# Performance work log

Measured on AMD Instinct MI355X. Metric: run time of the kernel, lower is better.

The kernel has to match this reference:

```python
import jax, jax.numpy as jnp
import numpy as np

N = 100000      # nodes
E = 1_600_000   # edges (avg degree 16)
DIMS = [(64, 64), (64, 64), (64, 40)]  # gnn_layers [64,64,64,40]


def setup_inputs() -> dict:
    key = jax.random.key(0)
    ks = jax.random.split(key, 2 + 3 * len(DIMS))
    inp = {
        "x": jax.random.normal(ks[0], (N, DIMS[0][0]), jnp.float32),
        "edge_index": jax.random.randint(ks[1], (2, E), 0, N),
    }
    k = 2
    for i, (din, dout) in enumerate(DIMS):
        s = 1.0 / np.sqrt(din)
        inp[f"Wl{i}"] = jax.random.uniform(ks[k], (din, dout), jnp.float32, -s, s); k += 1
        inp[f"bl{i}"] = jax.random.uniform(ks[k], (dout,), jnp.float32, -s, s); k += 1
        inp[f"Wr{i}"] = jax.random.uniform(ks[k], (din, dout), jnp.float32, -s, s); k += 1
    return inp


def _sage_conv(x, src, dst, Wl, bl, Wr):
    # PyG SAGEConv (mean aggr): out = lin_l(mean_{j in N(i)} x_j) + lin_r(x_i)
    deg = jax.ops.segment_sum(jnp.ones((src.shape[0],), x.dtype), dst, num_segments=N)
    agg = jax.ops.segment_sum(x[src], dst, num_segments=N)  # [N, din] scatter-add
    agg = agg / jnp.clip(deg, 1.0)[:, None]                  # mean; isolated nodes -> 0
    return agg @ Wl + bl + x @ Wr


def reference(x, edge_index, Wl0, bl0, Wr0, Wl1, bl1, Wr1, Wl2, bl2, Wr2):
    src, dst = edge_index[0], edge_index[1]
    h = x
    params = [(Wl0, bl0, Wr0), (Wl1, bl1, Wr1), (Wl2, bl2, Wr2)]
    for i, (Wl, bl, Wr) in enumerate(params):
        h = _sage_conv(h, src, dst, Wl, bl, Wr)
        if i != len(params) - 1:
            h = jax.nn.relu(h)
            # F.dropout with training=False is identity (eval mode)
    return jax.nn.log_softmax(h, axis=1)
```

## Files before the change

kernel.cpp:

```cpp
#include <hip/hip_runtime.h>
#include <math.h>

#define ACT_RELU 0
#define ACT_LSM  1
#define BSH 8
#define MAXNB 512

typedef __attribute__((ext_vector_type(8))) short bf16x8;
typedef __attribute__((ext_vector_type(4))) float f32x4;
typedef __attribute__((ext_vector_type(2))) float f32x2;

__device__ __forceinline__ unsigned f2bf(float f) {
  unsigned u = __float_as_uint(f);
  u += 0x7fffu + ((u >> 16) & 1u);
  return u >> 16;
}
template <bool HI>
__device__ __forceinline__ f32x2 f8cvt(unsigned w) {
  return __builtin_amdgcn_cvt_pk_f32_fp8((int)w, HI);
}
__device__ __forceinline__ unsigned char f2f8(float v) {
  return (unsigned char)(__builtin_amdgcn_cvt_pk_fp8_f32(v, v, 0, false) & 0xff);
}

__global__ void k_zero(int* __restrict__ p, int n) {
  int i = blockIdx.x * 256 + threadIdx.x;
  if (i < n) p[i] = 0;
}

__global__ void k_histB(const int* __restrict__ dst, int* __restrict__ bucket_cnt,
                        int E, int NB) {
  __shared__ int cntL[MAXNB];
  int t = threadIdx.x;
  for (int b = t; b < NB; b += 256) cntL[b] = 0;
  __syncthreads();
  int e0 = blockIdx.x * 4096;
  int e1 = min(e0 + 4096, E);
  for (int i = e0 + t; i < e1; i += 256) atomicAdd(&cntL[dst[i] >> BSH], 1);
  __syncthreads();
  for (int b = t; b < NB; b += 256)
    if (cntL[b]) atomicAdd(&bucket_cnt[b], cntL[b]);
}

__global__ void k_bscan(const int* __restrict__ bucket_cnt, int* __restrict__ bucket_base,
                        int* __restrict__ bucket_cursor, int NB) {
  __shared__ int sm[MAXNB];
  int t = threadIdx.x;
  sm[t] = (t < NB) ? bucket_cnt[t] : 0;
  __syncthreads();
  for (int off = 1; off < MAXNB; off <<= 1) {
    int x = (t >= off) ? sm[t - off] : 0;
    __syncthreads();
    sm[t] += x;
    __syncthreads();
  }
  int ex = (t == 0) ? 0 : sm[t - 1];
  if (t <= NB) bucket_base[t] = ex;
  if (t < NB) bucket_cursor[t] = ex;
}

__global__ void k_partition(const int* __restrict__ src, const int* __restrict__ dst,
                            int* __restrict__ bucket_cursor, int2* __restrict__ tmp,
                            int E, int NB) {
  __shared__ int cntL[MAXNB];
  __shared__ int baseL[MAXNB];
  int t = threadIdx.x;
  for (int b = t; b < NB; b += 256) cntL[b] = 0;
  __syncthreads();
  int e0 = blockIdx.x * 4096;
  int e1 = min(e0 + 4096, E);
  for (int i = e0 + t; i < e1; i += 256) atomicAdd(&cntL[dst[i] >> BSH], 1);
  __syncthreads();
  for (int b = t; b < NB; b += 256) {
    int c = cntL[b];
    baseL[b] = c ? atomicAdd(&bucket_cursor[b], c) : 0;
    cntL[b] = 0;
  }
  __syncthreads();
  for (int i = e0 + t; i < e1; i += 256) {
    int s = src[i], d = dst[i];
    int b = d >> BSH;
    int r = atomicAdd(&cntL[b], 1);
    tmp[baseL[b] + r] = make_int2(s, d);
  }
}

__global__ void __launch_bounds__(256) k_bmake(const int2* __restrict__ tmp,
                                               const int* __restrict__ bucket_base,
                                               int* __restrict__ row_ptr,
                                               int* __restrict__ edge_src,
                                               int N, int E, int NB) {
  __shared__ int cntL[256];
  __shared__ int scanL[256];
  int b = blockIdx.x;
  int t = threadIdx.x;
  int e0 = bucket_base[b], e1 = bucket_base[b + 1];
  cntL[t] = 0;
  __syncthreads();
  for (int i = e0 + t; i < e1; i += 256) atomicAdd(&cntL[tmp[i].y & 255], 1);
  __syncthreads();
  int v = cntL[t];
  scanL[t] = v;
  __syncthreads();
  for (int off = 1; off < 256; off <<= 1) {
    int x = (t >= off) ? scanL[t - off] : 0;
    __syncthreads();
    scanL[t] += x;
    __syncthreads();
  }
  int exc = scanL[t] - v;
  int node = (b << BSH) + t;
  if (node < N) row_ptr[node] = e0 + exc;
  if (b == NB - 1 && t == 0) row_ptr[N] = E;
  __syncthreads();
  cntL[t] = e0 + exc;
  __syncthreads();
  for (int i = e0 + t; i < e1; i += 256) {
    int2 e = tmp[i];
    int p = atomicAdd(&cntL[e.y & 255], 1);
    edge_src[p] = e.x;
  }
}

__global__ void k_hist(const int* __restrict__ dst, int* __restrict__ cnt, int E) {
  int i = blockIdx.x * blockDim.x + threadIdx.x;
  if (i < E) atomicAdd(&cnt[dst[i]], 1);
}

__global__ void k_scan_part(const int* __restrict__ cnt, int* __restrict__ bsum, int M) {
  __shared__ int sm[256];
  int t = threadIdx.x;
  int base = blockIdx.x * 2048 + t * 8;
  int s = 0;
#pragma unroll
  for (int j = 0; j < 8; ++j) { int i = base + j; if (i < M) s += cnt[i]; }
  sm[t] = s;
  __syncthreads();
  for (int off = 128; off > 0; off >>= 1) {
    if (t < off) sm[t] += sm[t + off];
    __syncthreads();
  }
  if (t == 0) bsum[blockIdx.x] = sm[0];
}

__global__ void k_scan_mid(const int* __restrict__ bsum, int* __restrict__ boff, int nb) {
  int l = threadIdx.x;
  int v = (l < nb) ? bsum[l] : 0;
  int inc = v;
  for (int off = 1; off < 64; off <<= 1) {
    int u = __shfl_up(inc, off);
    if (l >= off) inc += u;
  }
  if (l < nb) boff[l] = inc - v;
}

__global__ void k_scan_final(const int* __restrict__ cnt, const int* __restrict__ boff,
                             int* __restrict__ row_ptr, int* __restrict__ cursor, int M) {
  __shared__ int sm[256];
  int t = threadIdx.x;
  int base = blockIdx.x * 2048 + t * 8;
  int v[8];
  int s = 0;
#pragma unroll
  for (int j = 0; j < 8; ++j) { int i = base + j; v[j] = (i < M) ? cnt[i] : 0; s += v[j]; }
  sm[t] = s;
  __syncthreads();
  for (int off = 1; off < 256; off <<= 1) {
    int x = (t >= off) ? sm[t - off] : 0;
    __syncthreads();
    sm[t] += x;
    __syncthreads();
  }
  int run = boff[blockIdx.x] + sm[t] - s;
#pragma unroll
  for (int j = 0; j < 8; ++j) {
    int i = base + j;
    if (i < M) { row_ptr[i] = run; cursor[i] = run; }
    run += v[j];
  }
}

__global__ void k_fill(const int* __restrict__ src, const int* __restrict__ dst,
                       int* __restrict__ cursor, int* __restrict__ edge_src, int E) {
  int i = blockIdx.x * blockDim.x + threadIdx.x;
  if (i < E) {
    int d = dst[i];
    int p = atomicAdd(&cursor[d], 1);
    edge_src[p] = src[i];
  }
}

__global__ void __launch_bounds__(256) k_cast(const float* __restrict__ x,
                                              unsigned short* __restrict__ xb,
                                              unsigned char* __restrict__ x8, int n) {
  int i = blockIdx.x * 256 + threadIdx.x;
  if (i * 8 < n) {
    const float4* p = (const float4*)(x + (size_t)i * 8);
    float4 a = p[0], b = p[1];
    uint4 w;
    w.x = f2bf(a.x) | (f2bf(a.y) << 16);
    w.y = f2bf(a.z) | (f2bf(a.w) << 16);
    w.z = f2bf(b.x) | (f2bf(b.y) << 16);
    w.w = f2bf(b.z) | (f2bf(b.w) << 16);
    *(uint4*)(xb + (size_t)i * 8) = w;
    uint2 q;
    q.x = (unsigned)__builtin_amdgcn_cvt_pk_fp8_f32(a.x, a.y, 0, false);
    q.x = (unsigned)__builtin_amdgcn_cvt_pk_fp8_f32(a.z, a.w, (int)q.x, true);
    q.y = (unsigned)__builtin_amdgcn_cvt_pk_fp8_f32(b.x, b.y, 0, false);
    q.y = (unsigned)__builtin_amdgcn_cvt_pk_fp8_f32(b.z, b.w, (int)q.y, true);
    *(uint2*)(x8 + (size_t)i * 8) = q;
  }
}

#define MPAD 80

template <int DOUT, int ACT>
__global__ void __launch_bounds__(256) k_layer(const unsigned short* __restrict__ h,
                                               const unsigned char* __restrict__ h8,
                                               const int* __restrict__ row_ptr,
                                               const int* __restrict__ edge_src,
                                               const float* __restrict__ Wl,
                                               const float* __restrict__ Wr,
                                               const float* __restrict__ bias,
                                               void* __restrict__ outv,
                                               unsigned char* __restrict__ out8, int n) {
  constexpr int NT = (DOUT + 15) / 16;
  constexpr int PADN = NT * 16;
  __shared__ unsigned short Wlds[128 * PADN];
  __shared__ unsigned short meanL[4][16 * MPAD];
  int t = threadIdx.x;

  for (int fi = t; fi < 128 * PADN; fi += 256) {
    int k7 = fi & 7;
    int kb = (fi >> 3) & 3;
    int c16 = (fi >> 5) & 15;
    int rest = fi >> 9;
    int nt = rest % NT;
    int kb5 = rest / NT;
    int k = kb5 * 32 + kb * 8 + k7;
    int nn = nt * 16 + c16;
    float v = 0.f;
    if (nn < DOUT) v = (k < 64) ? Wl[k * DOUT + nn] : Wr[(k - 64) * DOUT + nn];
    Wlds[fi] = (unsigned short)f2bf(v);
  }

  int w = t >> 6, lane = t & 63;
  int r0 = (blockIdx.x * 4 + w) * 16;
  int g = lane & 7;
  int lb = lane & ~7;

  for (int half = 0; half < 2; ++half) {
    int node = half * 8 + (lane >> 3);
    int i = r0 + node;
    float a[8];
#pragma unroll
    for (int c = 0; c < 8; ++c) a[c] = 0.f;
    float scale = 0.f;
    if (i < n) {
      int rp0 = row_ptr[i], rp1 = row_ptr[i + 1];
      int deg = rp1 - rp0;
      scale = (deg > 0) ? (1.0f / (float)deg) : 0.f;
      for (int base = 0; base < deg; base += 8) {
        int idx = rp0 + base + g;
        int sv = (idx < rp1) ? edge_src[idx] : 0;
        int cnt = min(8, deg - base);
        uint2 v0, v1, v2, v3, v4, v5, v6, v7;
#pragma unroll
        for (int e = 0; e < 8; ++e) {
          int s = __shfl(sv, lb | e);
          const uint2* p = (const uint2*)(h8 + (size_t)s * 64) + g;
          if (e == 0 && e < cnt) v0 = *p;
          if (e == 1 && e < cnt) v1 = *p;
          if (e == 2 && e < cnt) v2 = *p;
          if (e == 3 && e < cnt) v3 = *p;
          if (e == 4 && e < cnt) v4 = *p;
          if (e == 5 && e < cnt) v5 = *p;
          if (e == 6 && e < cnt) v6 = *p;
          if (e == 7 && e < cnt) v7 = *p;
        }
#define ACCUM(vv, ee)                                                    \
        if ((ee) < cnt) {                                                \
          f32x2 p0 = f8cvt<false>(vv.x), p1 = f8cvt<true>(vv.x);         \
          f32x2 p2 = f8cvt<false>(vv.y), p3 = f8cvt<true>(vv.y);         \
          a[0] += p0.x; a[1] += p0.y; a[2] += p1.x; a[3] += p1.y;        \
          a[4] += p2.x; a[5] += p2.y; a[6] += p3.x; a[7] += p3.y;        \
        }
        ACCUM(v0, 0) ACCUM(v1, 1) ACCUM(v2, 2) ACCUM(v3, 3)
        ACCUM(v4, 4) ACCUM(v5, 5) ACCUM(v6, 6) ACCUM(v7, 7)
#undef ACCUM
      }
    }
    uint4 wv;
    wv.x = f2bf(a[0] * scale) | (f2bf(a[1] * scale) << 16);
    wv.y = f2bf(a[2] * scale) | (f2bf(a[3] * scale) << 16);
    wv.z = f2bf(a[4] * scale) | (f2bf(a[5] * scale) << 16);
    wv.w = f2bf(a[6] * scale) | (f2bf(a[7] * scale) << 16);
    *(uint4*)&meanL[w][node * MPAD + g * 8] = wv;
  }
  __syncthreads();

  int c = lane & 15;
  int kb = lane >> 4;
  bf16x8 bf[4][NT];
#pragma unroll
  for (int s = 0; s < 4; ++s)
#pragma unroll
    for (int nt = 0; nt < NT; ++nt)
      bf[s][nt] = *(const bf16x8*)&Wlds[(((s * NT + nt) * 16 + c) * 4 + kb) * 8];

  bf16x8 af[4];
  af[0] = *(const bf16x8*)&meanL[w][c * MPAD + kb * 8];
  af[1] = *(const bf16x8*)&meanL[w][c * MPAD + 32 + kb * 8];
  int row = r0 + c;
  if (row >= n) row = n - 1;
  size_t rb = (size_t)row * 64 + kb * 8;
  af[2] = *(const bf16x8*)(h + rb);
  af[3] = *(const bf16x8*)(h + rb + 32);

  f32x4 acc[NT];
#pragma unroll
  for (int nt = 0; nt < NT; ++nt) acc[nt] = (f32x4){0.f, 0.f, 0.f, 0.f};
#pragma unroll
  for (int s = 0; s < 4; ++s)
#pragma unroll
    for (int nt = 0; nt < NT; ++nt)
      acc[nt] = __builtin_amdgcn_mfma_f32_16x16x32_bf16(af[s], bf[s][nt], acc[nt], 0, 0, 0);

  int rbase = r0 + kb * 4;
  if (ACT == ACT_RELU) {
    unsigned short* out = (unsigned short*)outv;
#pragma unroll
    for (int nt = 0; nt < NT; ++nt) {
      float bval = bias[nt * 16 + c];
#pragma unroll
      for (int r = 0; r < 4; ++r) {
        int R = rbase + r;
        if (R < n) {
          float v = fmaxf(acc[nt][r] + bval, 0.f);
          size_t o = (size_t)R * DOUT + nt * 16 + c;
          out[o] = (unsigned short)f2bf(v);
          out8[o] = f2f8(v);
        }
      }
    }
  } else {
    float* out = (float*)outv;
    float bv[NT];
#pragma unroll
    for (int nt = 0; nt < NT; ++nt) bv[nt] = ((nt * 16 + c) < DOUT) ? bias[nt * 16 + c] : 0.f;
#pragma unroll
    for (int r = 0; r < 4; ++r) {
      int R = rbase + r;
      float v[NT];
      float m = -INFINITY;
#pragma unroll
      for (int nt = 0; nt < NT; ++nt) {
        bool valid = (nt * 16 + c) < DOUT;
        v[nt] = valid ? (acc[nt][r] + bv[nt]) : -INFINITY;
        m = fmaxf(m, v[nt]);
      }
#pragma unroll
      for (int off = 1; off < 16; off <<= 1) m = fmaxf(m, __shfl_xor(m, off));
      float es = 0.f;
#pragma unroll
      for (int nt = 0; nt < NT; ++nt)
        if ((nt * 16 + c) < DOUT) es += expf(v[nt] - m);
#pragma unroll
      for (int off = 1; off < 16; off <<= 1) es += __shfl_xor(es, off);
      float lse = logf(es);
      if (R < n) {
#pragma unroll
        for (int nt = 0; nt < NT; ++nt)
          if ((nt * 16 + c) < DOUT) out[(size_t)R * DOUT + nt * 16 + c] = v[nt] - m - lse;
      }
    }
  }
}

extern "C" void kernel_launch(void* const* d_in, const int* in_sizes, int n_in,
                              void* d_out, int out_size, void* d_ws, size_t ws_size,
                              hipStream_t stream) {
  const float* x   = (const float*)d_in[0];
  const int*   ei  = (const int*)d_in[1];
  const float* Wl0 = (const float*)d_in[2];
  const float* bl0 = (const float*)d_in[3];
  const float* Wr0 = (const float*)d_in[4];
  const float* Wl1 = (const float*)d_in[5];
  const float* bl1 = (const float*)d_in[6];
  const float* Wr1 = (const float*)d_in[7];
  const float* Wl2 = (const float*)d_in[8];
  const float* bl2 = (const float*)d_in[9];
  const float* Wr2 = (const float*)d_in[10];
  float* out = (float*)d_out;

  int N = in_sizes[0] / 64;
  int E = in_sizes[1] / 2;
  int M = N + 1;
  int NB = (N + 255) >> BSH;
  const int* src = ei;
  const int* dst = ei + E;

  char* p = (char*)d_ws;
  auto alloc = [&](size_t bytes) {
    char* r = p;
    p += (bytes + 255) & ~(size_t)255;
    return r;
  };
  int* cnt      = (int*)alloc((size_t)M * 4);
  int* row_ptr  = (int*)alloc((size_t)M * 4);
  int* cursor   = (int*)alloc((size_t)M * 4);
  int* bsum     = (int*)alloc(256 * 4);
  int* boff     = (int*)alloc(256 * 4);
  int* bk_cnt   = (int*)alloc((MAXNB + 1) * 4);
  int* bk_base  = (int*)alloc((MAXNB + 1) * 4);
  int* bk_cur   = (int*)alloc((MAXNB + 1) * 4);
  int* edge_src = (int*)alloc((size_t)E * 4);
  size_t szR1 = (size_t)E * 8 > (size_t)N * 128 ? (size_t)E * 8 : (size_t)N * 128;
  char* R1              = alloc(szR1);
  unsigned short* hbA   = (unsigned short*)alloc((size_t)N * 128);
  unsigned char*  P8A   = (unsigned char*)alloc((size_t)N * 64);
  unsigned char*  P8B   = (unsigned char*)alloc((size_t)N * 64);
  if ((size_t)(p - (char*)d_ws) > ws_size) return;

  bool bucketed = (NB <= MAXNB);
  int eb4 = (E + 4095) / 4096;

  if (bucketed) {
    k_zero<<<(MAXNB + 256) / 256, 256, 0, stream>>>(bk_cnt, MAXNB + 1);
    k_histB<<<eb4, 256, 0, stream>>>(dst, bk_cnt, E, NB);
    k_bscan<<<1, MAXNB, 0, stream>>>(bk_cnt, bk_base, bk_cur, NB);
    k_partition<<<eb4, 256, 0, stream>>>(src, dst, bk_cur, (int2*)R1, E, NB);
    k_bmake<<<NB, 256, 0, stream>>>((const int2*)R1, bk_base, row_ptr, edge_src, N, E, NB);
  } else {
    k_zero<<<(M + 255) / 256, 256, 0, stream>>>(cnt, M);
    k_hist<<<(E + 255) / 256, 256, 0, stream>>>(dst, cnt, E);
    int nb = (M + 2047) / 2048;
    k_scan_part<<<nb, 256, 0, stream>>>(cnt, bsum, M);
    k_scan_mid<<<1, 64, 0, stream>>>(bsum, boff, nb);
    k_scan_final<<<nb, 256, 0, stream>>>(cnt, boff, row_ptr, cursor, M);
    k_fill<<<(E + 255) / 256, 256, 0, stream>>>(src, dst, cursor, edge_src, E);
  }

  unsigned short* xb  = (unsigned short*)R1;
  unsigned short* hbB = (unsigned short*)R1;
  unsigned char*  x8  = P8A;
  unsigned char*  h8A = P8B;
  unsigned char*  h8B = P8A;

  int cb = (N * 64 / 8 + 255) / 256;
  int gb = (N + 63) / 64;

  k_cast<<<cb, 256, 0, stream>>>(x, xb, x8, N * 64);
  k_layer<64, ACT_RELU><<<gb, 256, 0, stream>>>(xb, x8, row_ptr, edge_src, Wl0, Wr0, bl0, hbA, h8A, N);
  k_layer<64, ACT_RELU><<<gb, 256, 0, stream>>>(hbA, h8A, row_ptr, edge_src, Wl1, Wr1, bl1, hbB, h8B, N);
  k_layer<40, ACT_LSM><<<gb, 256, 0, stream>>>(hbB, h8B, row_ptr, edge_src, Wl2, Wr2, bl2, out, nullptr, N);
}
```

Measured before the change: 221.8 us.

## Split fp8 feature table into two 32-column planes and gather per plane

The fp8 copy of node features is stored as two planes of 32 columns each instead of 64-byte rows. The gather loop now has 4 lanes per node covering all 16 nodes at once, and it runs two passes, one per plane. Each gathered row is 32 bytes, so the random-access working set per pass is halved, which is meant to improve L2/MALL hit rates. Nontemporal hints are added to streaming loads and stores, at the cost of reading the edge list twice.

```diff
diff --git a/kernel.cpp b/kernel.cpp
--- a/kernel.cpp
+++ b/kernel.cpp
@@ -9,6 +9,8 @@
 typedef __attribute__((ext_vector_type(8))) short bf16x8;
 typedef __attribute__((ext_vector_type(4))) float f32x4;
 typedef __attribute__((ext_vector_type(2))) float f32x2;
+typedef __attribute__((ext_vector_type(4))) unsigned int u32x4;
+typedef __attribute__((ext_vector_type(2))) unsigned int u32x2;
 
 __device__ __forceinline__ unsigned f2bf(float f) {
   unsigned u = __float_as_uint(f);
@@ -192,23 +194,30 @@
 
 __global__ void __launch_bounds__(256) k_cast(const float* __restrict__ x,
                                               unsigned short* __restrict__ xb,
-                                              unsigned char* __restrict__ x8, int n) {
+                                              unsigned char* __restrict__ x8, int node_n,
+                                              int n) {
   int i = blockIdx.x * 256 + threadIdx.x;
   if (i * 8 < n) {
-    const float4* p = (const float4*)(x + (size_t)i * 8);
-    float4 a = p[0], b = p[1];
-    uint4 w;
+    const f32x4* p = (const f32x4*)(x + (size_t)i * 8);
+    f32x4 a = __builtin_nontemporal_load(p);
+    f32x4 b = __builtin_nontemporal_load(p + 1);
+    u32x4 w;
     w.x = f2bf(a.x) | (f2bf(a.y) << 16);
     w.y = f2bf(a.z) | (f2bf(a.w) << 16);
     w.z = f2bf(b.x) | (f2bf(b.y) << 16);
     w.w = f2bf(b.z) | (f2bf(b.w) << 16);
-    *(uint4*)(xb + (size_t)i * 8) = w;
-    uint2 q;
+    __builtin_nontemporal_store(w, (u32x4*)(xb + (size_t)i * 8));
+    u32x2 q;
     q.x = (unsigned)__builtin_amdgcn_cvt_pk_fp8_f32(a.x, a.y, 0, false);
     q.x = (unsigned)__builtin_amdgcn_cvt_pk_fp8_f32(a.z, a.w, (int)q.x, true);
     q.y = (unsigned)__builtin_amdgcn_cvt_pk_fp8_f32(b.x, b.y, 0, false);
     q.y = (unsigned)__builtin_amdgcn_cvt_pk_fp8_f32(b.z, b.w, (int)q.y, true);
-    *(uint2*)(x8 + (size_t)i * 8) = q;
+    int node = i >> 3;
+    int d0 = (i & 7) * 8;
+    int plane = d0 >> 5;
+    int off = d0 & 31;
+    __builtin_nontemporal_store(q,
+        (u32x2*)(x8 + (size_t)plane * node_n * 32 + (size_t)node * 32 + off));
   }
 }
 
@@ -246,56 +255,62 @@
 
   int w = t >> 6, lane = t & 63;
   int r0 = (blockIdx.x * 4 + w) * 16;
-  int g = lane & 7;
-  int lb = lane & ~7;
-
-  for (int half = 0; half < 2; ++half) {
-    int node = half * 8 + (lane >> 3);
-    int i = r0 + node;
+  int node = lane >> 2;
+  int g = lane & 3;
+  int nb = lane & ~3;
+  int i = r0 + node;
+
+  int rp0 = 0, rp1 = 0, deg = 0;
+  float scale = 0.f;
+  if (i < n) {
+    rp0 = row_ptr[i];
+    rp1 = row_ptr[i + 1];
+    deg = rp1 - rp0;
+    scale = (deg > 0) ? (1.0f / (float)deg) : 0.f;
+  }
+
+  for (int p = 0; p < 2; ++p) {
+    const unsigned char* hp = h8 + (size_t)p * n * 32;
     float a[8];
 #pragma unroll
     for (int c = 0; c < 8; ++c) a[c] = 0.f;
-    float scale = 0.f;
-    if (i < n) {
-      int rp0 = row_ptr[i], rp1 = row_ptr[i + 1];
-      int deg = rp1 - rp0;
-      scale = (deg > 0) ? (1.0f / (float)deg) : 0.f;
-      for (int base = 0; base < deg; base += 8) {
-        int idx = rp0 + base + g;
-        int sv = (idx < rp1) ? edge_src[idx] : 0;
-        int cnt = min(8, deg - base);
-        uint2 v0, v1, v2, v3, v4, v5, v6, v7;
-#pragma unroll
-        for (int e = 0; e < 8; ++e) {
-          int s = __shfl(sv, lb | e);
-          const uint2* p = (const uint2*)(h8 + (size_t)s * 64) + g;
-          if (e == 0 && e < cnt) v0 = *p;
-          if (e == 1 && e < cnt) v1 = *p;
-          if (e == 2 && e < cnt) v2 = *p;
-          if (e == 3 && e < cnt) v3 = *p;
-          if (e == 4 && e < cnt) v4 = *p;
-          if (e == 5 && e < cnt) v5 = *p;
-          if (e == 6 && e < cnt) v6 = *p;
-          if (e == 7 && e < cnt) v7 = *p;
-        }
+    for (int base = 0; base < deg; base += 8) {
+      int ia = rp0 + base + g;
+      int ib = ia + 4;
+      int sva = (ia < rp1) ? __builtin_nontemporal_load(&edge_src[ia]) : 0;
+      int svb = (ib < rp1) ? __builtin_nontemporal_load(&edge_src[ib]) : 0;
+      int cnt = min(8, deg - base);
+      u32x2 v0, v1, v2, v3, v4, v5, v6, v7;
+#pragma unroll
+      for (int e = 0; e < 8; ++e) {
+        int s = __shfl((e < 4) ? sva : svb, nb | (e & 3));
+        const u32x2* ptr = (const u32x2*)(hp + (size_t)s * 32) + g;
+        if (e == 0 && e < cnt) v0 = *ptr;
+        if (e == 1 && e < cnt) v1 = *ptr;
+        if (e == 2 && e < cnt) v2 = *ptr;
+        if (e == 3 && e < cnt) v3 = *ptr;
+        if (e == 4 && e < cnt) v4 = *ptr;
+        if (e == 5 && e < cnt) v5 = *ptr;
+        if (e == 6 && e < cnt) v6 = *ptr;
+        if (e == 7 && e < cnt) v7 = *ptr;
+      }
 #define ACCUM(vv, ee)                                                    \
-        if ((ee) < cnt) {                                                \
-          f32x2 p0 = f8cvt<false>(vv.x), p1 = f8cvt<true>(vv.x);         \
-          f32x2 p2 = f8cvt<false>(vv.y), p3 = f8cvt<true>(vv.y);         \
-          a[0] += p0.x; a[1] += p0.y; a[2] += p1.x; a[3] += p1.y;        \
-          a[4] += p2.x; a[5] += p2.y; a[6] += p3.x; a[7] += p3.y;        \
-        }
-        ACCUM(v0, 0) ACCUM(v1, 1) ACCUM(v2, 2) ACCUM(v3, 3)
-        ACCUM(v4, 4) ACCUM(v5, 5) ACCUM(v6, 6) ACCUM(v7, 7)
+      if ((ee) < cnt) {                                                  \
+        f32x2 p0 = f8cvt<false>(vv.x), p1 = f8cvt<true>(vv.x);           \
+        f32x2 p2 = f8cvt<false>(vv.y), p3 = f8cvt<true>(vv.y);           \
+        a[0] += p0.x; a[1] += p0.y; a[2] += p1.x; a[3] += p1.y;          \
+        a[4] += p2.x; a[5] += p2.y; a[6] += p3.x; a[7] += p3.y;          \
+      }
+      ACCUM(v0, 0) ACCUM(v1, 1) ACCUM(v2, 2) ACCUM(v3, 3)
+      ACCUM(v4, 4) ACCUM(v5, 5) ACCUM(v6, 6) ACCUM(v7, 7)
 #undef ACCUM
-      }
     }
-    uint4 wv;
+    u32x4 wv;
     wv.x = f2bf(a[0] * scale) | (f2bf(a[1] * scale) << 16);
     wv.y = f2bf(a[2] * scale) | (f2bf(a[3] * scale) << 16);
     wv.z = f2bf(a[4] * scale) | (f2bf(a[5] * scale) << 16);
     wv.w = f2bf(a[6] * scale) | (f2bf(a[7] * scale) << 16);
-    *(uint4*)&meanL[w][node * MPAD + g * 8] = wv;
+    *(u32x4*)&meanL[w][node * MPAD + p * 32 + g * 8] = wv;
   }
   __syncthreads();
 
@@ -314,8 +329,8 @@
   int row = r0 + c;
   if (row >= n) row = n - 1;
   size_t rb = (size_t)row * 64 + kb * 8;
-  af[2] = *(const bf16x8*)(h + rb);
-  af[3] = *(const bf16x8*)(h + rb + 32);
+  af[2] = __builtin_nontemporal_load((const bf16x8*)(h + rb));
+  af[3] = __builtin_nontemporal_load((const bf16x8*)(h + rb + 32));
 
   f32x4 acc[NT];
 #pragma unroll
@@ -332,14 +347,17 @@
 #pragma unroll
     for (int nt = 0; nt < NT; ++nt) {
       float bval = bias[nt * 16 + c];
+      int col = nt * 16 + c;
+      int plane = col >> 5, colp = col & 31;
 #pragma unroll
       for (int r = 0; r < 4; ++r) {
         int R = rbase + r;
         if (R < n) {
           float v = fmaxf(acc[nt][r] + bval, 0.f);
-          size_t o = (size_t)R * DOUT + nt * 16 + c;
-          out[o] = (unsigned short)f2bf(v);
-          out8[o] = f2f8(v);
+          __builtin_nontemporal_store((unsigned short)f2bf(v),
+                                      out + (size_t)R * DOUT + col);
+          __builtin_nontemporal_store(f2f8(v),
+                                      out8 + ((size_t)plane * n + R) * 32 + colp);
         }
       }
     }
@@ -371,7 +389,9 @@
       if (R < n) {
 #pragma unroll
         for (int nt = 0; nt < NT; ++nt)
-          if ((nt * 16 + c) < DOUT) out[(size_t)R * DOUT + nt * 16 + c] = v[nt] - m - lse;
+          if ((nt * 16 + c) < DOUT)
+            __builtin_nontemporal_store(v[nt] - m - lse,
+                                        out + (size_t)R * DOUT + nt * 16 + c);
       }
     }
   }
@@ -450,7 +470,7 @@
   int cb = (N * 64 / 8 + 255) / 256;
   int gb = (N + 63) / 64;
 
-  k_cast<<<cb, 256, 0, stream>>>(x, xb, x8, N * 64);
+  k_cast<<<cb, 256, 0, stream>>>(x, xb, x8, N, N * 64);
   k_layer<64, ACT_RELU><<<gb, 256, 0, stream>>>(xb, x8, row_ptr, edge_src, Wl0, Wr0, bl0, hbA, h8A, N);
   k_layer<64, ACT_RELU><<<gb, 256, 0, stream>>>(hbA, h8A, row_ptr, edge_src, Wl1, Wr1, bl1, hbB, h8B, N);
   k_layer<40, ACT_LSM><<<gb, 256, 0, stream>>>(hbB, h8B, row_ptr, edge_src, Wl2, Wr2, bl2, out, nullptr, N);
```

Measured after the change: 290.1 us. +30.8%, slower.
